# Kernel tuning notes

Hardware: AMD Instinct MI355X
Metric: run time of the kernel (lower is better)

## Reference

```python
import jax, jax.numpy as jnp
import numpy as np
from jax.ops import segment_sum

N_NODES = 50000
N_EDGES = 800000
HIDDEN = 96
N_CLASSES = 10
N_GRAPHS = 64


def gcn_conv(x, W, b, src, dst, num_nodes):
    """PyG GCNConv: symmetric-normalized aggregation with self-loops.
    out = D^{-1/2} (A + I) D^{-1/2} (x W) + b, with D the degree of A + I.
    Self-loop contribution handled analytically instead of appending edges.
    """
    ones = jnp.ones((src.shape[0],), dtype=x.dtype)
    deg = segment_sum(ones, dst, num_segments=num_nodes) + 1.0  # +1 for self-loop
    dinv = jax.lax.rsqrt(deg)
    h = x @ W  # [N, H] small GEMM
    norm = dinv[src] * dinv[dst]  # [E]
    msg = h[src] * norm[:, None]  # [E, H] dominant gather
    out = segment_sum(msg, dst, num_segments=num_nodes)  # scatter-add
    out = out + h * (dinv * dinv)[:, None]  # self-loop term
    return out + b


def setup_inputs() -> dict:
    key = jax.random.key(0)
    ks = jax.random.split(key, 12)
    x = jax.random.normal(ks[0], (N_NODES, HIDDEN), dtype=jnp.float32)
    edge_index = jax.random.randint(ks[1], (2, N_EDGES), 0, N_NODES, dtype=jnp.int64)
    batch = jnp.sort(jax.random.randint(ks[2], (N_NODES,), 0, N_GRAPHS, dtype=jnp.int64))
    s = 1.0 / np.sqrt(HIDDEN)
    W0 = jax.random.normal(ks[3], (HIDDEN, HIDDEN), dtype=jnp.float32) * s
    b0 = jnp.zeros((HIDDEN,), dtype=jnp.float32)
    W1 = jax.random.normal(ks[4], (HIDDEN, HIDDEN), dtype=jnp.float32) * s
    b1 = jnp.zeros((HIDDEN,), dtype=jnp.float32)
    W2 = jax.random.normal(ks[5], (HIDDEN, HIDDEN), dtype=jnp.float32) * s
    b2 = jnp.zeros((HIDDEN,), dtype=jnp.float32)
    W_lin = jax.random.normal(ks[6], (HIDDEN, N_CLASSES), dtype=jnp.float32) * s
    b_lin = jnp.zeros((N_CLASSES,), dtype=jnp.float32)
    return {"x": x, "edge_index": edge_index, "batch": batch,
            "W0": W0, "b0": b0, "W1": W1, "b1": b1, "W2": W2, "b2": b2,
            "W_lin": W_lin, "b_lin": b_lin}


def reference(x, edge_index, batch, W0, b0, W1, b1, W2, b2, W_lin, b_lin):
    src, dst = edge_index[0], edge_index[1]
    n = x.shape[0]
    h = jax.nn.relu(gcn_conv(x, W0, b0, src, dst, n))
    h = jax.nn.relu(gcn_conv(h, W1, b1, src, dst, n))
    h = gcn_conv(h, W2, b2, src, dst, n)  # last layer: no activation
    # global_mean_pool over batch index
    sums = segment_sum(h, batch, num_segments=N_GRAPHS)  # [G, H]
    cnts = segment_sum(jnp.ones((n,), dtype=h.dtype), batch, num_segments=N_GRAPHS)
    pooled = sums / jnp.maximum(cnts, 1.0)[:, None]
    # dropout is identity in eval mode
    return pooled @ W_lin + b_lin  # [G, num_classes]
```

## Files before the change

### kernel.cpp

```cpp
#include <hip/hip_runtime.h>
#include <hip/hip_bf16.h>

#define HID 96
#define NGRAPHS 64
#define SENT 0xC3C3u
#define NROWS 50116

typedef __attribute__((ext_vector_type(8))) short short8;
typedef __attribute__((ext_vector_type(4))) float floatx4;
typedef __attribute__((ext_vector_type(8))) unsigned short ushort8v;

__device__ __forceinline__ float bf16_to_f32(unsigned short u) {
    unsigned int v = ((unsigned int)u) << 16;
    return __builtin_bit_cast(float, v);
}
__device__ __forceinline__ unsigned short f32_to_bf16(float f) {
    unsigned int u = __builtin_bit_cast(unsigned int, f);
    u += 0x7fff + ((u >> 16) & 1);
    return (unsigned short)(u >> 16);
}

__device__ __forceinline__ void gather_batch(const unsigned short* __restrict__ h,
                                             const unsigned short* __restrict__ csr,
                                             int i, int fi, float& a0, float& a1) {
    ushort8v iv = *(const ushort8v*)(csr + i);
    ushort2 v0 = *(const ushort2*)(h + (size_t)iv[0] * HID + fi);
    ushort2 v1 = *(const ushort2*)(h + (size_t)iv[1] * HID + fi);
    ushort2 v2 = *(const ushort2*)(h + (size_t)iv[2] * HID + fi);
    ushort2 v3 = *(const ushort2*)(h + (size_t)iv[3] * HID + fi);
    ushort2 v4 = *(const ushort2*)(h + (size_t)iv[4] * HID + fi);
    ushort2 v5 = *(const ushort2*)(h + (size_t)iv[5] * HID + fi);
    ushort2 v6 = *(const ushort2*)(h + (size_t)iv[6] * HID + fi);
    ushort2 v7 = *(const ushort2*)(h + (size_t)iv[7] * HID + fi);
    a0 += bf16_to_f32(v0.x) + bf16_to_f32(v1.x) + bf16_to_f32(v2.x) +
          bf16_to_f32(v3.x) + bf16_to_f32(v4.x) + bf16_to_f32(v5.x) +
          bf16_to_f32(v6.x) + bf16_to_f32(v7.x);
    a1 += bf16_to_f32(v0.y) + bf16_to_f32(v1.y) + bf16_to_f32(v2.y) +
          bf16_to_f32(v3.y) + bf16_to_f32(v4.y) + bf16_to_f32(v5.y) +
          bf16_to_f32(v6.y) + bf16_to_f32(v7.y);
}

__device__ __forceinline__ void gather2(const unsigned short* __restrict__ h,
                                        const unsigned short* __restrict__ csr,
                                        int i0, int e0, int i1, int e1, int fi,
                                        float& a00, float& a01, float& a10,
                                        float& a11) {
    while (i0 < e0 && i1 < e1) {
        ushort8v ca = *(const ushort8v*)(csr + i0);
        ushort8v cb = *(const ushort8v*)(csr + i1);
        i0 += 8;
        i1 += 8;
        ushort2 u0 = *(const ushort2*)(h + (size_t)ca[0] * HID + fi);
        ushort2 u1 = *(const ushort2*)(h + (size_t)ca[1] * HID + fi);
        ushort2 u2 = *(const ushort2*)(h + (size_t)ca[2] * HID + fi);
        ushort2 u3 = *(const ushort2*)(h + (size_t)ca[3] * HID + fi);
        ushort2 u4 = *(const ushort2*)(h + (size_t)ca[4] * HID + fi);
        ushort2 u5 = *(const ushort2*)(h + (size_t)ca[5] * HID + fi);
        ushort2 u6 = *(const ushort2*)(h + (size_t)ca[6] * HID + fi);
        ushort2 u7 = *(const ushort2*)(h + (size_t)ca[7] * HID + fi);
        ushort2 w0 = *(const ushort2*)(h + (size_t)cb[0] * HID + fi);
        ushort2 w1 = *(const ushort2*)(h + (size_t)cb[1] * HID + fi);
        ushort2 w2 = *(const ushort2*)(h + (size_t)cb[2] * HID + fi);
        ushort2 w3 = *(const ushort2*)(h + (size_t)cb[3] * HID + fi);
        ushort2 w4 = *(const ushort2*)(h + (size_t)cb[4] * HID + fi);
        ushort2 w5 = *(const ushort2*)(h + (size_t)cb[5] * HID + fi);
        ushort2 w6 = *(const ushort2*)(h + (size_t)cb[6] * HID + fi);
        ushort2 w7 = *(const ushort2*)(h + (size_t)cb[7] * HID + fi);
        a00 += bf16_to_f32(u0.x) + bf16_to_f32(u1.x) + bf16_to_f32(u2.x) +
               bf16_to_f32(u3.x) + bf16_to_f32(u4.x) + bf16_to_f32(u5.x) +
               bf16_to_f32(u6.x) + bf16_to_f32(u7.x);
        a01 += bf16_to_f32(u0.y) + bf16_to_f32(u1.y) + bf16_to_f32(u2.y) +
               bf16_to_f32(u3.y) + bf16_to_f32(u4.y) + bf16_to_f32(u5.y) +
               bf16_to_f32(u6.y) + bf16_to_f32(u7.y);
        a10 += bf16_to_f32(w0.x) + bf16_to_f32(w1.x) + bf16_to_f32(w2.x) +
               bf16_to_f32(w3.x) + bf16_to_f32(w4.x) + bf16_to_f32(w5.x) +
               bf16_to_f32(w6.x) + bf16_to_f32(w7.x);
        a11 += bf16_to_f32(w0.y) + bf16_to_f32(w1.y) + bf16_to_f32(w2.y) +
               bf16_to_f32(w3.y) + bf16_to_f32(w4.y) + bf16_to_f32(w5.y) +
               bf16_to_f32(w6.y) + bf16_to_f32(w7.y);
    }
    for (; i0 < e0; i0 += 8) gather_batch(h, csr, i0, fi, a00, a01);
    for (; i1 < e1; i1 += 8) gather_batch(h, csr, i1, fi, a10, a11);
}

__global__ __launch_bounds__(256) void init_kernel(
    int* __restrict__ deg, float* __restrict__ psum,
    unsigned short* __restrict__ bufA, unsigned short* __restrict__ bufB, int N) {
    int i = blockIdx.x * 256 + threadIdx.x;
    if (i < N) deg[i] = 0;
    if (i < NGRAPHS * HID + NGRAPHS) psum[i] = 0.0f;
    if (i < HID) {
        bufA[(size_t)SENT * HID + i] = 0;
        bufB[(size_t)SENT * HID + i] = 0;
    }
}

__global__ void deg_kernel(const int* __restrict__ dst, int* __restrict__ deg,
                           int n_edges) {
    int t = blockIdx.x * blockDim.x + threadIdx.x;
    int e0 = t * 4;
    if (e0 + 4 <= n_edges) {
        int4 d4 = *(const int4*)(dst + e0);
        atomicAdd(&deg[d4.x], 1);
        atomicAdd(&deg[d4.y], 1);
        atomicAdd(&deg[d4.z], 1);
        atomicAdd(&deg[d4.w], 1);
    } else {
        for (int e = e0; e < n_edges; e++) atomicAdd(&deg[dst[e]], 1);
    }
}

__global__ __launch_bounds__(256) void scan_phaseA(const int* __restrict__ deg,
                                                   float* __restrict__ dinv,
                                                   int* __restrict__ blocksum,
                                                   int N) {
    int i = blockIdx.x * 256 + threadIdx.x;
    int d = (i < N) ? deg[i] : 0;
    if (i < N) dinv[i] = rsqrtf((float)d + 1.0f);
    int v = (d + 7) & ~7;
#pragma unroll
    for (int off = 32; off > 0; off >>= 1) v += __shfl_down(v, off, 64);
    __shared__ int s[4];
    if ((threadIdx.x & 63) == 0) s[threadIdx.x >> 6] = v;
    __syncthreads();
    if (threadIdx.x == 0) blocksum[blockIdx.x] = s[0] + s[1] + s[2] + s[3];
}

__global__ __launch_bounds__(256) void scan_phaseC(const int* __restrict__ deg,
                                                   const int* __restrict__ blocksum,
                                                   int* __restrict__ rowptr,
                                                   int* __restrict__ cursor,
                                                   int N, int NB) {
    int t = threadIdx.x;
    int mine = (t < NB && t < blockIdx.x) ? blocksum[t] : 0;
#pragma unroll
    for (int off = 32; off > 0; off >>= 1) mine += __shfl_down(mine, off, 64);
    __shared__ int ps[4];
    if ((t & 63) == 0) ps[t >> 6] = mine;
    __syncthreads();
    int pref = ps[0] + ps[1] + ps[2] + ps[3];

    __shared__ int s[256];
    int i = blockIdx.x * 256 + t;
    int own = (i < N) ? (deg[i] + 7) & ~7 : 0;
    s[t] = own;
    __syncthreads();
#pragma unroll
    for (int off = 1; off < 256; off <<= 1) {
        int v = (t >= off) ? s[t - off] : 0;
        __syncthreads();
        s[t] += v;
        __syncthreads();
    }
    if (i < N) {
        int r = pref + s[t] - own;
        rowptr[i] = r;
        cursor[i] = r;
        if (i == N - 1) rowptr[N] = r + own;
    }
}

__global__ void csr_fill(const int* __restrict__ src, const int* __restrict__ dst,
                         int* __restrict__ cursor,
                         unsigned short* __restrict__ csr_src, int n_edges) {
    int t = blockIdx.x * blockDim.x + threadIdx.x;
    int e0 = t * 8;
    if (e0 + 8 <= n_edges) {
        int4 da = *(const int4*)(dst + e0);
        int4 db = *(const int4*)(dst + e0 + 4);
        int4 sa = *(const int4*)(src + e0);
        int4 sb = *(const int4*)(src + e0 + 4);
        int p0 = atomicAdd(&cursor[da.x], 1);
        int p1 = atomicAdd(&cursor[da.y], 1);
        int p2 = atomicAdd(&cursor[da.z], 1);
        int p3 = atomicAdd(&cursor[da.w], 1);
        int p4 = atomicAdd(&cursor[db.x], 1);
        int p5 = atomicAdd(&cursor[db.y], 1);
        int p6 = atomicAdd(&cursor[db.z], 1);
        int p7 = atomicAdd(&cursor[db.w], 1);
        csr_src[p0] = (unsigned short)sa.x;
        csr_src[p1] = (unsigned short)sa.y;
        csr_src[p2] = (unsigned short)sa.z;
        csr_src[p3] = (unsigned short)sa.w;
        csr_src[p4] = (unsigned short)sb.x;
        csr_src[p5] = (unsigned short)sb.y;
        csr_src[p6] = (unsigned short)sb.z;
        csr_src[p7] = (unsigned short)sb.w;
    } else {
        for (int e = e0; e < n_edges; e++) {
            int p = atomicAdd(&cursor[dst[e]], 1);
            csr_src[p] = (unsigned short)src[e];
        }
    }
}

__global__ void swizzle_W(const float* __restrict__ W0, const float* __restrict__ W1,
                          const float* __restrict__ W2, unsigned short* __restrict__ Wz) {
    const float* W = (blockIdx.x == 0) ? W0 : (blockIdx.x == 1) ? W1 : W2;
    unsigned short* dst = Wz + blockIdx.x * HID * HID;
    for (int e = threadIdx.x; e < HID * HID; e += blockDim.x) {
        int k = e / HID, n = e % HID;
        int nt = n >> 4, kki = k >> 5, quad = (k >> 3) & 3, j = k & 7;
        int lane = (n & 15) | (quad << 4);
        dst[(((nt * 3 + kki) * 64 + lane) << 3) | j] = f32_to_bf16(W[e]);
    }
}

__global__ __launch_bounds__(256) void gemm0_f32(
    const float* __restrict__ X, const unsigned short* __restrict__ Wz,
    const float* __restrict__ dinv, unsigned short* __restrict__ Out, int Mtiles) {
    int wv = threadIdx.x >> 6;
    int lane = threadIdx.x & 63;
    int quad = lane >> 4;
    int mrow = lane & 15;
    int tt = blockIdx.x * 2 + (wv >> 1);
    int half = wv & 1;
    if (tt >= Mtiles) return;

    short8 bfrag[9];
    const short8* Wz8 = (const short8*)Wz;
#pragma unroll
    for (int f = 0; f < 9; f++) bfrag[f] = Wz8[(half * 9 + f) * 64 + lane];

    int m0 = tt * 16;
    const float* arow = X + (size_t)(m0 + mrow) * HID + quad * 8;
    short8 a[3];
#pragma unroll
    for (int kb = 0; kb < 3; kb++) {
        float4 u = *(const float4*)(arow + kb * 32);
        float4 v = *(const float4*)(arow + kb * 32 + 4);
        short8 t;
        t[0] = (short)f32_to_bf16(u.x); t[1] = (short)f32_to_bf16(u.y);
        t[2] = (short)f32_to_bf16(u.z); t[3] = (short)f32_to_bf16(u.w);
        t[4] = (short)f32_to_bf16(v.x); t[5] = (short)f32_to_bf16(v.y);
        t[6] = (short)f32_to_bf16(v.z); t[7] = (short)f32_to_bf16(v.w);
        a[kb] = t;
    }
    float dscale[4];
#pragma unroll
    for (int r = 0; r < 4; r++) dscale[r] = dinv[m0 + quad * 4 + r];
    unsigned short* orow = Out + (size_t)m0 * HID;
#pragma unroll
    for (int ntl = 0; ntl < 3; ntl++) {
        int nt = half * 3 + ntl;
        floatx4 c = {0.0f, 0.0f, 0.0f, 0.0f};
        c = __builtin_amdgcn_mfma_f32_16x16x32_bf16(a[0], bfrag[ntl * 3 + 0], c, 0, 0, 0);
        c = __builtin_amdgcn_mfma_f32_16x16x32_bf16(a[1], bfrag[ntl * 3 + 1], c, 0, 0, 0);
        c = __builtin_amdgcn_mfma_f32_16x16x32_bf16(a[2], bfrag[ntl * 3 + 2], c, 0, 0, 0);
#pragma unroll
        for (int r = 0; r < 4; r++)
            orow[(size_t)(quad * 4 + r) * HID + nt * 16 + mrow] =
                f32_to_bf16(c[r] * dscale[r]);
    }
}

__global__ __launch_bounds__(256) void fused_gather_gemm(
    const unsigned short* __restrict__ h, const int* __restrict__ rowptr,
    const unsigned short* __restrict__ csr, const float* __restrict__ dinv,
    const float* __restrict__ bias, const unsigned short* __restrict__ Wz,
    unsigned short* __restrict__ Out, int Mtiles) {
    __shared__ unsigned short tile[2][16][104];
    int wv = threadIdx.x >> 6;
    int lane = threadIdx.x & 63;
    int quad = lane >> 4;
    int mrow = lane & 15;
    int tsel = wv >> 1;
    int half = wv & 1;
    int tt = blockIdx.x * 2 + tsel;
    bool active = tt < Mtiles;
    int fi = (lane < 48) ? lane * 2 : 94;

    if (active) {
        float b0 = bias[fi], b1 = bias[fi + 1];
        int n0 = tt * 16;
        for (int jj = 0; jj < 8; jj += 2) {
            int j0 = half * 8 + jj;
            int na = n0 + j0;
            int nb = na + 1;
            int ia = rowptr[na];
            int ea = rowptr[na + 1];
            int ib = ea;
            int eb = rowptr[nb + 1];
            float da = dinv[na], db = dinv[nb];
            ushort2 ha = *(const ushort2*)(h + (size_t)na * HID + fi);
            ushort2 hb = *(const ushort2*)(h + (size_t)nb * HID + fi);
            float a00 = bf16_to_f32(ha.x), a01 = bf16_to_f32(ha.y);
            float a10 = bf16_to_f32(hb.x), a11 = bf16_to_f32(hb.y);
            gather2(h, csr, ia, ea, ib, eb, fi, a00, a01, a10, a11);
            a00 = fmaxf(a00 * da + b0, 0.0f);
            a01 = fmaxf(a01 * da + b1, 0.0f);
            a10 = fmaxf(a10 * db + b0, 0.0f);
            a11 = fmaxf(a11 * db + b1, 0.0f);
            if (lane < 48) {
                tile[tsel][j0][fi] = f32_to_bf16(a00);
                tile[tsel][j0][fi + 1] = f32_to_bf16(a01);
                tile[tsel][j0 + 1][fi] = f32_to_bf16(a10);
                tile[tsel][j0 + 1][fi + 1] = f32_to_bf16(a11);
            }
        }
    }
    __syncthreads();
    if (!active) return;

    short8 bfrag[9];
    const short8* Wz8 = (const short8*)Wz;
#pragma unroll
    for (int f = 0; f < 9; f++) bfrag[f] = Wz8[(half * 9 + f) * 64 + lane];

    const unsigned short* tp = &tile[tsel][0][0];
    short8 a[3];
#pragma unroll
    for (int kb = 0; kb < 3; kb++)
        a[kb] = *(const short8*)(tp + mrow * 104 + quad * 8 + kb * 32);
    int n0 = tt * 16;
    float dscale[4];
#pragma unroll
    for (int r = 0; r < 4; r++) dscale[r] = dinv[n0 + quad * 4 + r];
    unsigned short* orow = Out + (size_t)n0 * HID;
#pragma unroll
    for (int ntl = 0; ntl < 3; ntl++) {
        int nt = half * 3 + ntl;
        floatx4 c = {0.0f, 0.0f, 0.0f, 0.0f};
        c = __builtin_amdgcn_mfma_f32_16x16x32_bf16(a[0], bfrag[ntl * 3 + 0], c, 0, 0, 0);
        c = __builtin_amdgcn_mfma_f32_16x16x32_bf16(a[1], bfrag[ntl * 3 + 1], c, 0, 0, 0);
        c = __builtin_amdgcn_mfma_f32_16x16x32_bf16(a[2], bfrag[ntl * 3 + 2], c, 0, 0, 0);
#pragma unroll
        for (int r = 0; r < 4; r++)
            orow[(size_t)(quad * 4 + r) * HID + nt * 16 + mrow] =
                f32_to_bf16(c[r] * dscale[r]);
    }
}

__global__ __launch_bounds__(256) void gather_pool(
    const unsigned short* __restrict__ h, const int* __restrict__ rowptr,
    const unsigned short* __restrict__ csr, const float* __restrict__ dinv,
    const float* __restrict__ bias, const int* __restrict__ batch,
    float* __restrict__ psum, float* __restrict__ pcnt, int Ntiles8) {
    int wv = threadIdx.x >> 6;
    int lane = threadIdx.x & 63;
    int tt = blockIdx.x * 4 + wv;
    if (tt >= Ntiles8) return;
    int fi = (lane < 48) ? lane * 2 : 94;
    float b0 = bias[fi], b1 = bias[fi + 1];

    int n0 = tt * 8;
    int g_cur = batch[n0];
    float s0 = 0.0f, s1 = 0.0f;
    int cnt = 0;
    for (int jj = 0; jj < 8; jj += 2) {
        int na = n0 + jj;
        int nb = na + 1;
        int ia = rowptr[na];
        int ea = rowptr[na + 1];
        int ib = ea;
        int eb = rowptr[nb + 1];
        float da = dinv[na], db = dinv[nb];
        ushort2 ha = *(const ushort2*)(h + (size_t)na * HID + fi);
        ushort2 hb = *(const ushort2*)(h + (size_t)nb * HID + fi);
        float a00 = bf16_to_f32(ha.x), a01 = bf16_to_f32(ha.y);
        float a10 = bf16_to_f32(hb.x), a11 = bf16_to_f32(hb.y);
        gather2(h, csr, ia, ea, ib, eb, fi, a00, a01, a10, a11);
        a00 = a00 * da + b0;
        a01 = a01 * da + b1;
        a10 = a10 * db + b0;
        a11 = a11 * db + b1;
        int ga = batch[na];
        if (ga != g_cur) {
            if (lane < 48) {
                atomicAdd(&psum[g_cur * HID + fi], s0);
                atomicAdd(&psum[g_cur * HID + fi + 1], s1);
            }
            if (lane == 0) atomicAdd(&pcnt[g_cur], (float)cnt);
            s0 = 0.0f; s1 = 0.0f; cnt = 0;
            g_cur = ga;
        }
        s0 += a00; s1 += a01; cnt++;
        int gb = batch[nb];
        if (gb != g_cur) {
            if (lane < 48) {
                atomicAdd(&psum[g_cur * HID + fi], s0);
                atomicAdd(&psum[g_cur * HID + fi + 1], s1);
            }
            if (lane == 0) atomicAdd(&pcnt[g_cur], (float)cnt);
            s0 = 0.0f; s1 = 0.0f; cnt = 0;
            g_cur = gb;
        }
        s0 += a10; s1 += a11; cnt++;
    }
    if (lane < 48) {
        atomicAdd(&psum[g_cur * HID + fi], s0);
        atomicAdd(&psum[g_cur * HID + fi + 1], s1);
    }
    if (lane == 0) atomicAdd(&pcnt[g_cur], (float)cnt);
}

__global__ __launch_bounds__(640) void final_kernel(
    const float* __restrict__ sums, const float* __restrict__ cnts,
    const float* __restrict__ Wlin, const float* __restrict__ blin,
    float* __restrict__ out) {
    int t = threadIdx.x;
    if (t >= NGRAPHS * 10) return;
    int g = t / 10;
    int c = t % 10;
    float denom = fmaxf(cnts[g], 1.0f);
    float acc = blin[c];
#pragma unroll
    for (int f = 0; f < HID; f++)
        acc += (sums[g * HID + f] / denom) * Wlin[f * 10 + c];
    out[t] = acc;
}

extern "C" void kernel_launch(void* const* d_in, const int* in_sizes, int n_in,
                              void* d_out, int out_size, void* d_ws,
                              size_t ws_size, hipStream_t stream) {
    const float* x = (const float*)d_in[0];
    const int* edge = (const int*)d_in[1];
    const int* batch = (const int*)d_in[2];
    const float* W[3] = {(const float*)d_in[3], (const float*)d_in[5],
                         (const float*)d_in[7]};
    const float* B[3] = {(const float*)d_in[4], (const float*)d_in[6],
                         (const float*)d_in[8]};
    const float* Wlin = (const float*)d_in[9];
    const float* blin = (const float*)d_in[10];
    float* out = (float*)d_out;

    int N = in_sizes[0] / HID;
    int E = in_sizes[1] / 2;
    const int* src = edge;
    const int* dst = edge + E;
    int NB = (N + 255) / 256;

    char* ws = (char*)d_ws;
    size_t off = 0;
    auto alloc = [&](size_t bytes) {
        void* p = ws + off;
        off += (bytes + 255) & ~(size_t)255;
        return p;
    };
    int* deg = (int*)alloc((size_t)N * 4);
    float* dinv = (float*)alloc((size_t)N * 4);
    int* rowptr = (int*)alloc(((size_t)N + 1) * 4);
    int* cursor = (int*)alloc((size_t)N * 4);
    int* blocksum = (int*)alloc((size_t)NB * 4);
    size_t csr_cap = (size_t)E + 8 * (size_t)N;
    unsigned short* csr_src = (unsigned short*)alloc(csr_cap * 2 + 64);
    unsigned short* Wz = (unsigned short*)alloc(3 * HID * HID * 2);
    unsigned short* bufA = (unsigned short*)alloc((size_t)NROWS * HID * 2);
    unsigned short* bufB = (unsigned short*)alloc((size_t)NROWS * HID * 2);
    float* psum = (float*)alloc((NGRAPHS * HID + NGRAPHS) * 4);
    float* pcnt = psum + NGRAPHS * HID;

    hipMemsetAsync(csr_src, 0xC3, csr_cap * 2, stream);
    init_kernel<<<NB, 256, 0, stream>>>(deg, psum, bufA, bufB, N);
    deg_kernel<<<(E / 4 + 255) / 256, 256, 0, stream>>>(dst, deg, E);
    scan_phaseA<<<NB, 256, 0, stream>>>(deg, dinv, blocksum, N);
    scan_phaseC<<<NB, 256, 0, stream>>>(deg, blocksum, rowptr, cursor, N, NB);
    csr_fill<<<(E / 8 + 255) / 256, 256, 0, stream>>>(src, dst, cursor, csr_src, E);
    swizzle_W<<<3, 256, 0, stream>>>(W[0], W[1], W[2], Wz);

    int Mtiles = (N + 15) / 16;
    int grid2 = (Mtiles + 1) / 2;
    int Ntiles8 = (N + 7) / 8;
    int gridp = (Ntiles8 + 3) / 4;

    gemm0_f32<<<grid2, 256, 0, stream>>>(x, Wz, dinv, bufA, Mtiles);
    fused_gather_gemm<<<grid2, 256, 0, stream>>>(
        bufA, rowptr, csr_src, dinv, B[0], Wz + 1 * HID * HID, bufB, Mtiles);
    fused_gather_gemm<<<grid2, 256, 0, stream>>>(
        bufB, rowptr, csr_src, dinv, B[1], Wz + 2 * HID * HID, bufA, Mtiles);
    gather_pool<<<gridp, 256, 0, stream>>>(bufA, rowptr, csr_src, dinv, B[2],
                                           batch, psum, pcnt, Ntiles8);
    final_kernel<<<1, 640, 0, stream>>>(psum, pcnt, Wlin, blin, out);
}
```

Baseline: 307.8 us.

## Slice feature buffers into 12-column panels and split gather from GEMM

Stores the bf16 node features as 8 column slices of 12 features each (slice-major), so each gather block works on one slice of about 1.2 MB that can stay cache-resident during the random neighbour gather. The fused gather+GEMM and gather+pool kernels become separate gather_sliced, gemm_sliced and pool_sliced kernels. The aim is a better cache hit rate for the irregular row accesses. In exchange there are more launches, the CSR indices are read 8 times, and intermediate activations make an extra round trip through memory.

```diff
diff --git a/kernel.cpp b/kernel.cpp
--- a/kernel.cpp
+++ b/kernel.cpp
@@ -5,6 +5,7 @@
 #define NGRAPHS 64
 #define SENT 0xC3C3u
 #define NROWS 50116
+#define NPB 84
 
 typedef __attribute__((ext_vector_type(8))) short short8;
 typedef __attribute__((ext_vector_type(4))) float floatx4;
@@ -18,69 +19,6 @@
     unsigned int u = __builtin_bit_cast(unsigned int, f);
     u += 0x7fff + ((u >> 16) & 1);
     return (unsigned short)(u >> 16);
-}
-
-__device__ __forceinline__ void gather_batch(const unsigned short* __restrict__ h,
-                                             const unsigned short* __restrict__ csr,
-                                             int i, int fi, float& a0, float& a1) {
-    ushort8v iv = *(const ushort8v*)(csr + i);
-    ushort2 v0 = *(const ushort2*)(h + (size_t)iv[0] * HID + fi);
-    ushort2 v1 = *(const ushort2*)(h + (size_t)iv[1] * HID + fi);
-    ushort2 v2 = *(const ushort2*)(h + (size_t)iv[2] * HID + fi);
-    ushort2 v3 = *(const ushort2*)(h + (size_t)iv[3] * HID + fi);
-    ushort2 v4 = *(const ushort2*)(h + (size_t)iv[4] * HID + fi);
-    ushort2 v5 = *(const ushort2*)(h + (size_t)iv[5] * HID + fi);
-    ushort2 v6 = *(const ushort2*)(h + (size_t)iv[6] * HID + fi);
-    ushort2 v7 = *(const ushort2*)(h + (size_t)iv[7] * HID + fi);
-    a0 += bf16_to_f32(v0.x) + bf16_to_f32(v1.x) + bf16_to_f32(v2.x) +
-          bf16_to_f32(v3.x) + bf16_to_f32(v4.x) + bf16_to_f32(v5.x) +
-          bf16_to_f32(v6.x) + bf16_to_f32(v7.x);
-    a1 += bf16_to_f32(v0.y) + bf16_to_f32(v1.y) + bf16_to_f32(v2.y) +
-          bf16_to_f32(v3.y) + bf16_to_f32(v4.y) + bf16_to_f32(v5.y) +
-          bf16_to_f32(v6.y) + bf16_to_f32(v7.y);
-}
-
-__device__ __forceinline__ void gather2(const unsigned short* __restrict__ h,
-                                        const unsigned short* __restrict__ csr,
-                                        int i0, int e0, int i1, int e1, int fi,
-                                        float& a00, float& a01, float& a10,
-                                        float& a11) {
-    while (i0 < e0 && i1 < e1) {
-        ushort8v ca = *(const ushort8v*)(csr + i0);
-        ushort8v cb = *(const ushort8v*)(csr + i1);
-        i0 += 8;
-        i1 += 8;
-        ushort2 u0 = *(const ushort2*)(h + (size_t)ca[0] * HID + fi);
-        ushort2 u1 = *(const ushort2*)(h + (size_t)ca[1] * HID + fi);
-        ushort2 u2 = *(const ushort2*)(h + (size_t)ca[2] * HID + fi);
-        ushort2 u3 = *(const ushort2*)(h + (size_t)ca[3] * HID + fi);
-        ushort2 u4 = *(const ushort2*)(h + (size_t)ca[4] * HID + fi);
-        ushort2 u5 = *(const ushort2*)(h + (size_t)ca[5] * HID + fi);
-        ushort2 u6 = *(const ushort2*)(h + (size_t)ca[6] * HID + fi);
-        ushort2 u7 = *(const ushort2*)(h + (size_t)ca[7] * HID + fi);
-        ushort2 w0 = *(const ushort2*)(h + (size_t)cb[0] * HID + fi);
-        ushort2 w1 = *(const ushort2*)(h + (size_t)cb[1] * HID + fi);
-        ushort2 w2 = *(const ushort2*)(h + (size_t)cb[2] * HID + fi);
-        ushort2 w3 = *(const ushort2*)(h + (size_t)cb[3] * HID + fi);
-        ushort2 w4 = *(const ushort2*)(h + (size_t)cb[4] * HID + fi);
-        ushort2 w5 = *(const ushort2*)(h + (size_t)cb[5] * HID + fi);
-        ushort2 w6 = *(const ushort2*)(h + (size_t)cb[6] * HID + fi);
-        ushort2 w7 = *(const ushort2*)(h + (size_t)cb[7] * HID + fi);
-        a00 += bf16_to_f32(u0.x) + bf16_to_f32(u1.x) + bf16_to_f32(u2.x) +
-               bf16_to_f32(u3.x) + bf16_to_f32(u4.x) + bf16_to_f32(u5.x) +
-               bf16_to_f32(u6.x) + bf16_to_f32(u7.x);
-        a01 += bf16_to_f32(u0.y) + bf16_to_f32(u1.y) + bf16_to_f32(u2.y) +
-               bf16_to_f32(u3.y) + bf16_to_f32(u4.y) + bf16_to_f32(u5.y) +
-               bf16_to_f32(u6.y) + bf16_to_f32(u7.y);
-        a10 += bf16_to_f32(w0.x) + bf16_to_f32(w1.x) + bf16_to_f32(w2.x) +
-               bf16_to_f32(w3.x) + bf16_to_f32(w4.x) + bf16_to_f32(w5.x) +
-               bf16_to_f32(w6.x) + bf16_to_f32(w7.x);
-        a11 += bf16_to_f32(w0.y) + bf16_to_f32(w1.y) + bf16_to_f32(w2.y) +
-               bf16_to_f32(w3.y) + bf16_to_f32(w4.y) + bf16_to_f32(w5.y) +
-               bf16_to_f32(w6.y) + bf16_to_f32(w7.y);
-    }
-    for (; i0 < e0; i0 += 8) gather_batch(h, csr, i0, fi, a00, a01);
-    for (; i1 < e1; i1 += 8) gather_batch(h, csr, i1, fi, a10, a11);
 }
 
 __global__ __launch_bounds__(256) void init_kernel(
@@ -90,8 +28,9 @@
     if (i < N) deg[i] = 0;
     if (i < NGRAPHS * HID + NGRAPHS) psum[i] = 0.0f;
     if (i < HID) {
-        bufA[(size_t)SENT * HID + i] = 0;
-        bufB[(size_t)SENT * HID + i] = 0;
+        size_t off = ((size_t)(i / 12) * NROWS + SENT) * 12 + (i % 12);
+        bufA[off] = 0;
+        bufB[off] = 0;
     }
 }
 
@@ -239,7 +178,6 @@
     float dscale[4];
 #pragma unroll
     for (int r = 0; r < 4; r++) dscale[r] = dinv[m0 + quad * 4 + r];
-    unsigned short* orow = Out + (size_t)m0 * HID;
 #pragma unroll
     for (int ntl = 0; ntl < 3; ntl++) {
         int nt = half * 3 + ntl;
@@ -247,76 +185,47 @@
         c = __builtin_amdgcn_mfma_f32_16x16x32_bf16(a[0], bfrag[ntl * 3 + 0], c, 0, 0, 0);
         c = __builtin_amdgcn_mfma_f32_16x16x32_bf16(a[1], bfrag[ntl * 3 + 1], c, 0, 0, 0);
         c = __builtin_amdgcn_mfma_f32_16x16x32_bf16(a[2], bfrag[ntl * 3 + 2], c, 0, 0, 0);
+        int f = nt * 16 + mrow;
+        unsigned short* ocol = Out + (size_t)(f / 12) * NROWS * 12 + (f % 12);
 #pragma unroll
         for (int r = 0; r < 4; r++)
-            orow[(size_t)(quad * 4 + r) * HID + nt * 16 + mrow] =
-                f32_to_bf16(c[r] * dscale[r]);
-    }
-}
-
-__global__ __launch_bounds__(256) void fused_gather_gemm(
-    const unsigned short* __restrict__ h, const int* __restrict__ rowptr,
-    const unsigned short* __restrict__ csr, const float* __restrict__ dinv,
-    const float* __restrict__ bias, const unsigned short* __restrict__ Wz,
-    unsigned short* __restrict__ Out, int Mtiles) {
-    __shared__ unsigned short tile[2][16][104];
+            ocol[(size_t)(m0 + quad * 4 + r) * 12] = f32_to_bf16(c[r] * dscale[r]);
+    }
+}
+
+__global__ __launch_bounds__(256) void gemm_sliced(
+    const unsigned short* __restrict__ A, const unsigned short* __restrict__ Wz,
+    const float* __restrict__ dinv, unsigned short* __restrict__ Out, int Mtiles) {
     int wv = threadIdx.x >> 6;
     int lane = threadIdx.x & 63;
     int quad = lane >> 4;
     int mrow = lane & 15;
-    int tsel = wv >> 1;
+    int tt = blockIdx.x * 2 + (wv >> 1);
     int half = wv & 1;
-    int tt = blockIdx.x * 2 + tsel;
-    bool active = tt < Mtiles;
-    int fi = (lane < 48) ? lane * 2 : 94;
-
-    if (active) {
-        float b0 = bias[fi], b1 = bias[fi + 1];
-        int n0 = tt * 16;
-        for (int jj = 0; jj < 8; jj += 2) {
-            int j0 = half * 8 + jj;
-            int na = n0 + j0;
-            int nb = na + 1;
-            int ia = rowptr[na];
-            int ea = rowptr[na + 1];
-            int ib = ea;
-            int eb = rowptr[nb + 1];
-            float da = dinv[na], db = dinv[nb];
-            ushort2 ha = *(const ushort2*)(h + (size_t)na * HID + fi);
-            ushort2 hb = *(const ushort2*)(h + (size_t)nb * HID + fi);
-            float a00 = bf16_to_f32(ha.x), a01 = bf16_to_f32(ha.y);
-            float a10 = bf16_to_f32(hb.x), a11 = bf16_to_f32(hb.y);
-            gather2(h, csr, ia, ea, ib, eb, fi, a00, a01, a10, a11);
-            a00 = fmaxf(a00 * da + b0, 0.0f);
-            a01 = fmaxf(a01 * da + b1, 0.0f);
-            a10 = fmaxf(a10 * db + b0, 0.0f);
-            a11 = fmaxf(a11 * db + b1, 0.0f);
-            if (lane < 48) {
-                tile[tsel][j0][fi] = f32_to_bf16(a00);
-                tile[tsel][j0][fi + 1] = f32_to_bf16(a01);
-                tile[tsel][j0 + 1][fi] = f32_to_bf16(a10);
-                tile[tsel][j0 + 1][fi + 1] = f32_to_bf16(a11);
-            }
-        }
-    }
-    __syncthreads();
-    if (!active) return;
+    if (tt >= Mtiles) return;
 
     short8 bfrag[9];
     const short8* Wz8 = (const short8*)Wz;
 #pragma unroll
     for (int f = 0; f < 9; f++) bfrag[f] = Wz8[(half * 9 + f) * 64 + lane];
 
-    const unsigned short* tp = &tile[tsel][0][0];
+    int m0 = tt * 16;
+    int m = m0 + mrow;
     short8 a[3];
 #pragma unroll
-    for (int kb = 0; kb < 3; kb++)
-        a[kb] = *(const short8*)(tp + mrow * 104 + quad * 8 + kb * 32);
-    int n0 = tt * 16;
+    for (int kb = 0; kb < 3; kb++) {
+        int c = quad * 8 + kb * 32;
+        int c4 = c + 4;
+        ushort4 lo = *(const ushort4*)(A + ((size_t)(c / 12) * NROWS + m) * 12 + (c % 12));
+        ushort4 hi = *(const ushort4*)(A + ((size_t)(c4 / 12) * NROWS + m) * 12 + (c4 % 12));
+        short8 t;
+        t[0] = (short)lo.x; t[1] = (short)lo.y; t[2] = (short)lo.z; t[3] = (short)lo.w;
+        t[4] = (short)hi.x; t[5] = (short)hi.y; t[6] = (short)hi.z; t[7] = (short)hi.w;
+        a[kb] = t;
+    }
     float dscale[4];
 #pragma unroll
-    for (int r = 0; r < 4; r++) dscale[r] = dinv[n0 + quad * 4 + r];
-    unsigned short* orow = Out + (size_t)n0 * HID;
+    for (int r = 0; r < 4; r++) dscale[r] = dinv[m0 + quad * 4 + r];
 #pragma unroll
     for (int ntl = 0; ntl < 3; ntl++) {
         int nt = half * 3 + ntl;
@@ -324,74 +233,116 @@
         c = __builtin_amdgcn_mfma_f32_16x16x32_bf16(a[0], bfrag[ntl * 3 + 0], c, 0, 0, 0);
         c = __builtin_amdgcn_mfma_f32_16x16x32_bf16(a[1], bfrag[ntl * 3 + 1], c, 0, 0, 0);
         c = __builtin_amdgcn_mfma_f32_16x16x32_bf16(a[2], bfrag[ntl * 3 + 2], c, 0, 0, 0);
+        int f = nt * 16 + mrow;
+        unsigned short* ocol = Out + (size_t)(f / 12) * NROWS * 12 + (f % 12);
 #pragma unroll
         for (int r = 0; r < 4; r++)
-            orow[(size_t)(quad * 4 + r) * HID + nt * 16 + mrow] =
-                f32_to_bf16(c[r] * dscale[r]);
-    }
-}
-
-__global__ __launch_bounds__(256) void gather_pool(
+            ocol[(size_t)(m0 + quad * 4 + r) * 12] = f32_to_bf16(c[r] * dscale[r]);
+    }
+}
+
+__global__ __launch_bounds__(256) void gather_sliced(
     const unsigned short* __restrict__ h, const int* __restrict__ rowptr,
     const unsigned short* __restrict__ csr, const float* __restrict__ dinv,
-    const float* __restrict__ bias, const int* __restrict__ batch,
-    float* __restrict__ psum, float* __restrict__ pcnt, int Ntiles8) {
+    const float* __restrict__ bias, unsigned short* __restrict__ outa,
+    int N, int do_relu) {
+    int s = blockIdx.x & 7;
+    int tile = blockIdx.x >> 3;
     int wv = threadIdx.x >> 6;
     int lane = threadIdx.x & 63;
-    int tt = blockIdx.x * 4 + wv;
-    if (tt >= Ntiles8) return;
-    int fi = (lane < 48) ? lane * 2 : 94;
-    float b0 = bias[fi], b1 = bias[fi + 1];
-
-    int n0 = tt * 8;
-    int g_cur = batch[n0];
-    float s0 = 0.0f, s1 = 0.0f;
-    int cnt = 0;
-    for (int jj = 0; jj < 8; jj += 2) {
-        int na = n0 + jj;
-        int nb = na + 1;
-        int ia = rowptr[na];
-        int ea = rowptr[na + 1];
-        int ib = ea;
-        int eb = rowptr[nb + 1];
-        float da = dinv[na], db = dinv[nb];
-        ushort2 ha = *(const ushort2*)(h + (size_t)na * HID + fi);
-        ushort2 hb = *(const ushort2*)(h + (size_t)nb * HID + fi);
-        float a00 = bf16_to_f32(ha.x), a01 = bf16_to_f32(ha.y);
-        float a10 = bf16_to_f32(hb.x), a11 = bf16_to_f32(hb.y);
-        gather2(h, csr, ia, ea, ib, eb, fi, a00, a01, a10, a11);
-        a00 = a00 * da + b0;
-        a01 = a01 * da + b1;
-        a10 = a10 * db + b0;
-        a11 = a11 * db + b1;
-        int ga = batch[na];
-        if (ga != g_cur) {
-            if (lane < 48) {
-                atomicAdd(&psum[g_cur * HID + fi], s0);
-                atomicAdd(&psum[g_cur * HID + fi + 1], s1);
-            }
-            if (lane == 0) atomicAdd(&pcnt[g_cur], (float)cnt);
-            s0 = 0.0f; s1 = 0.0f; cnt = 0;
-            g_cur = ga;
+    int sub = lane / 3;
+    int r = lane - sub * 3;
+    if (sub >= 21) return;
+    int n = tile * NPB + wv * 21 + sub;
+    if (n >= N) return;
+
+    const unsigned short* hs = h + (size_t)s * NROWS * 12;
+    int fo = r * 4;
+    int start = rowptr[n];
+    int end = rowptr[n + 1];
+    float di = dinv[n];
+
+    ushort4 hv = *(const ushort4*)(hs + (size_t)n * 12 + fo);
+    float a0 = bf16_to_f32(hv.x), a1 = bf16_to_f32(hv.y);
+    float a2 = bf16_to_f32(hv.z), a3 = bf16_to_f32(hv.w);
+
+    for (int i = start; i < end; i += 8) {
+        ushort8v iv = *(const ushort8v*)(csr + i);
+        ushort4 v0 = *(const ushort4*)(hs + (size_t)iv[0] * 12 + fo);
+        ushort4 v1 = *(const ushort4*)(hs + (size_t)iv[1] * 12 + fo);
+        ushort4 v2 = *(const ushort4*)(hs + (size_t)iv[2] * 12 + fo);
+        ushort4 v3 = *(const ushort4*)(hs + (size_t)iv[3] * 12 + fo);
+        ushort4 v4 = *(const ushort4*)(hs + (size_t)iv[4] * 12 + fo);
+        ushort4 v5 = *(const ushort4*)(hs + (size_t)iv[5] * 12 + fo);
+        ushort4 v6 = *(const ushort4*)(hs + (size_t)iv[6] * 12 + fo);
+        ushort4 v7 = *(const ushort4*)(hs + (size_t)iv[7] * 12 + fo);
+        a0 += bf16_to_f32(v0.x) + bf16_to_f32(v1.x) + bf16_to_f32(v2.x) +
+              bf16_to_f32(v3.x) + bf16_to_f32(v4.x) + bf16_to_f32(v5.x) +
+              bf16_to_f32(v6.x) + bf16_to_f32(v7.x);
+        a1 += bf16_to_f32(v0.y) + bf16_to_f32(v1.y) + bf16_to_f32(v2.y) +
+              bf16_to_f32(v3.y) + bf16_to_f32(v4.y) + bf16_to_f32(v5.y) +
+              bf16_to_f32(v6.y) + bf16_to_f32(v7.y);
+        a2 += bf16_to_f32(v0.z) + bf16_to_f32(v1.z) + bf16_to_f32(v2.z) +
+              bf16_to_f32(v3.z) + bf16_to_f32(v4.z) + bf16_to_f32(v5.z) +
+              bf16_to_f32(v6.z) + bf16_to_f32(v7.z);
+        a3 += bf16_to_f32(v0.w) + bf16_to_f32(v1.w) + bf16_to_f32(v2.w) +
+              bf16_to_f32(v3.w) + bf16_to_f32(v4.w) + bf16_to_f32(v5.w) +
+              bf16_to_f32(v6.w) + bf16_to_f32(v7.w);
+    }
+    float4 bb = *(const float4*)(bias + s * 12 + fo);
+    a0 = a0 * di + bb.x;
+    a1 = a1 * di + bb.y;
+    a2 = a2 * di + bb.z;
+    a3 = a3 * di + bb.w;
+    if (do_relu) {
+        a0 = fmaxf(a0, 0.0f);
+        a1 = fmaxf(a1, 0.0f);
+        a2 = fmaxf(a2, 0.0f);
+        a3 = fmaxf(a3, 0.0f);
+    }
+    ushort4 o;
+    o.x = f32_to_bf16(a0);
+    o.y = f32_to_bf16(a1);
+    o.z = f32_to_bf16(a2);
+    o.w = f32_to_bf16(a3);
+    *(ushort4*)(outa + (size_t)s * NROWS * 12 + (size_t)n * 12 + fo) = o;
+}
+
+#define PCH 32
+__global__ __launch_bounds__(96) void pool_sliced(
+    const unsigned short* __restrict__ a3, const int* __restrict__ batch,
+    float* __restrict__ sums, float* __restrict__ cnts, int N) {
+    int n0 = blockIdx.x * PCH;
+    if (n0 >= N) return;
+    int f = threadIdx.x;
+    const unsigned short* col = a3 + (size_t)(f / 12) * NROWS * 12 + (f % 12);
+    int nend = min(n0 + PCH, N);
+    int gfirst = batch[n0];
+    int glast = batch[nend - 1];
+    if (gfirst == glast) {
+        float acc = 0.0f;
+#pragma unroll 8
+        for (int n = n0; n < nend; n++) acc += bf16_to_f32(col[(size_t)n * 12]);
+        atomicAdd(&sums[gfirst * HID + f], acc);
+        if (f == 0) atomicAdd(&cnts[gfirst], (float)(nend - n0));
+        return;
+    }
+    int g_cur = gfirst;
+    float acc = 0.0f, cacc = 0.0f;
+    for (int n = n0; n < nend; n++) {
+        int g = batch[n];
+        if (g != g_cur) {
+            atomicAdd(&sums[g_cur * HID + f], acc);
+            if (f == 0) atomicAdd(&cnts[g_cur], cacc);
+            acc = 0.0f;
+            cacc = 0.0f;
+            g_cur = g;
         }
-        s0 += a00; s1 += a01; cnt++;
-        int gb = batch[nb];
-        if (gb != g_cur) {
-            if (lane < 48) {
-                atomicAdd(&psum[g_cur * HID + fi], s0);
-                atomicAdd(&psum[g_cur * HID + fi + 1], s1);
-            }
-            if (lane == 0) atomicAdd(&pcnt[g_cur], (float)cnt);
-            s0 = 0.0f; s1 = 0.0f; cnt = 0;
-            g_cur = gb;
-        }
-        s0 += a10; s1 += a11; cnt++;
-    }
-    if (lane < 48) {
-        atomicAdd(&psum[g_cur * HID + fi], s0);
-        atomicAdd(&psum[g_cur * HID + fi + 1], s1);
-    }
-    if (lane == 0) atomicAdd(&pcnt[g_cur], (float)cnt);
+        acc += bf16_to_f32(col[(size_t)n * 12]);
+        cacc += 1.0f;
+    }
+    atomicAdd(&sums[g_cur * HID + f], acc);
+    if (f == 0) atomicAdd(&cnts[g_cur], cacc);
 }
 
 __global__ __launch_bounds__(640) void final_kernel(
@@ -460,15 +411,21 @@
 
     int Mtiles = (N + 15) / 16;
     int grid2 = (Mtiles + 1) / 2;
-    int Ntiles8 = (N + 7) / 8;
-    int gridp = (Ntiles8 + 3) / 4;
+    int gtiles = (N + NPB - 1) / NPB;
+    int ggrid = 8 * gtiles;
+    int pgrid = (N + PCH - 1) / PCH;
 
     gemm0_f32<<<grid2, 256, 0, stream>>>(x, Wz, dinv, bufA, Mtiles);
-    fused_gather_gemm<<<grid2, 256, 0, stream>>>(
-        bufA, rowptr, csr_src, dinv, B[0], Wz + 1 * HID * HID, bufB, Mtiles);
-    fused_gather_gemm<<<grid2, 256, 0, stream>>>(
-        bufB, rowptr, csr_src, dinv, B[1], Wz + 2 * HID * HID, bufA, Mtiles);
-    gather_pool<<<gridp, 256, 0, stream>>>(bufA, rowptr, csr_src, dinv, B[2],
-                                           batch, psum, pcnt, Ntiles8);
+    gather_sliced<<<ggrid, 256, 0, stream>>>(bufA, rowptr, csr_src, dinv, B[0],
+                                             bufB, N, 1);
+    gemm_sliced<<<grid2, 256, 0, stream>>>(bufB, Wz + 1 * HID * HID, dinv, bufA,
+                                           Mtiles);
+    gather_sliced<<<ggrid, 256, 0, stream>>>(bufA, rowptr, csr_src, dinv, B[1],
+                                             bufB, N, 1);
+    gemm_sliced<<<grid2, 256, 0, stream>>>(bufB, Wz + 2 * HID * HID, dinv, bufA,
+                                           Mtiles);
+    gather_sliced<<<ggrid, 256, 0, stream>>>(bufA, rowptr, csr_src, dinv, B[2],
+                                             bufB, N, 0);
+    pool_sliced<<<pgrid, 96, 0, stream>>>(bufB, batch, psum, pcnt, N);
     final_kernel<<<1, 640, 0, stream>>>(psum, pcnt, Wlin, blin, out);
 }
```

New measurement: 344.2 us. +11.8%, slower.

## Feature-slice last-layer features per XCC for cache-local gather-pool

Applied to the files above, without the earlier changes.

The second fused layer now writes its output in a sliced layout: eight column slices of 12 features, each stored contiguously over all rows. The final gather+pool kernel becomes a persistent kernel with per-slice atomic work queues. Each block starts on the slice matching its XCC ID so that slice's working set (about 1.2 MB) stays in that XCC's L2, and gathers 8-byte feature chunks per neighbor. This targets the random-gather L2 miss traffic, at the cost of eight passes over the CSR and rowptr, more atomics into psum, and strided scattered writes in the layer-2 epilogue.

```diff
diff --git a/kernel.cpp b/kernel.cpp
--- a/kernel.cpp
+++ b/kernel.cpp
@@ -5,6 +5,7 @@
 #define NGRAPHS 64
 #define SENT 0xC3C3u
 #define NROWS 50116
+#define NPT 1344
 
 typedef __attribute__((ext_vector_type(8))) short short8;
 typedef __attribute__((ext_vector_type(4))) float floatx4;
@@ -84,14 +85,17 @@
 }
 
 __global__ __launch_bounds__(256) void init_kernel(
-    int* __restrict__ deg, float* __restrict__ psum,
-    unsigned short* __restrict__ bufA, unsigned short* __restrict__ bufB, int N) {
+    int* __restrict__ deg, float* __restrict__ psum, int* __restrict__ queues,
+    unsigned short* __restrict__ bufA, unsigned short* __restrict__ bufB,
+    unsigned short* __restrict__ bufC, int N) {
     int i = blockIdx.x * 256 + threadIdx.x;
     if (i < N) deg[i] = 0;
     if (i < NGRAPHS * HID + NGRAPHS) psum[i] = 0.0f;
+    if (i < 8) queues[i] = 0;
     if (i < HID) {
         bufA[(size_t)SENT * HID + i] = 0;
         bufB[(size_t)SENT * HID + i] = 0;
+        bufC[((size_t)(i / 12) * NROWS + SENT) * 12 + (i % 12)] = 0;
     }
 }
 
@@ -258,7 +262,7 @@
     const unsigned short* __restrict__ h, const int* __restrict__ rowptr,
     const unsigned short* __restrict__ csr, const float* __restrict__ dinv,
     const float* __restrict__ bias, const unsigned short* __restrict__ Wz,
-    unsigned short* __restrict__ Out, int Mtiles) {
+    unsigned short* __restrict__ Out, int Mtiles, int sliced_out) {
     __shared__ unsigned short tile[2][16][104];
     int wv = threadIdx.x >> 6;
     int lane = threadIdx.x & 63;
@@ -316,7 +320,6 @@
     float dscale[4];
 #pragma unroll
     for (int r = 0; r < 4; r++) dscale[r] = dinv[n0 + quad * 4 + r];
-    unsigned short* orow = Out + (size_t)n0 * HID;
 #pragma unroll
     for (int ntl = 0; ntl < 3; ntl++) {
         int nt = half * 3 + ntl;
@@ -324,74 +327,116 @@
         c = __builtin_amdgcn_mfma_f32_16x16x32_bf16(a[0], bfrag[ntl * 3 + 0], c, 0, 0, 0);
         c = __builtin_amdgcn_mfma_f32_16x16x32_bf16(a[1], bfrag[ntl * 3 + 1], c, 0, 0, 0);
         c = __builtin_amdgcn_mfma_f32_16x16x32_bf16(a[2], bfrag[ntl * 3 + 2], c, 0, 0, 0);
-#pragma unroll
-        for (int r = 0; r < 4; r++)
-            orow[(size_t)(quad * 4 + r) * HID + nt * 16 + mrow] =
-                f32_to_bf16(c[r] * dscale[r]);
-    }
-}
-
-__global__ __launch_bounds__(256) void gather_pool(
+        int f = nt * 16 + mrow;
+        if (sliced_out) {
+            unsigned short* ocol = Out + ((size_t)(f / 12) * NROWS) * 12 + (f % 12);
+#pragma unroll
+            for (int r = 0; r < 4; r++)
+                ocol[(size_t)(n0 + quad * 4 + r) * 12] = f32_to_bf16(c[r] * dscale[r]);
+        } else {
+            unsigned short* orow = Out + (size_t)n0 * HID;
+#pragma unroll
+            for (int r = 0; r < 4; r++)
+                orow[(size_t)(quad * 4 + r) * HID + f] = f32_to_bf16(c[r] * dscale[r]);
+        }
+    }
+}
+
+__global__ __launch_bounds__(256) void gather_pool_sliced(
     const unsigned short* __restrict__ h, const int* __restrict__ rowptr,
     const unsigned short* __restrict__ csr, const float* __restrict__ dinv,
     const float* __restrict__ bias, const int* __restrict__ batch,
-    float* __restrict__ psum, float* __restrict__ pcnt, int Ntiles8) {
+    float* __restrict__ psum, float* __restrict__ pcnt,
+    int* __restrict__ queues, int N, int Ntiles) {
+    int xcc;
+    asm volatile("s_getreg_b32 %0, hwreg(HW_REG_XCC_ID)" : "=s"(xcc));
+    xcc &= 7;
+    __shared__ int tile_s;
     int wv = threadIdx.x >> 6;
     int lane = threadIdx.x & 63;
-    int tt = blockIdx.x * 4 + wv;
-    if (tt >= Ntiles8) return;
-    int fi = (lane < 48) ? lane * 2 : 94;
-    float b0 = bias[fi], b1 = bias[fi + 1];
-
-    int n0 = tt * 8;
-    int g_cur = batch[n0];
-    float s0 = 0.0f, s1 = 0.0f;
-    int cnt = 0;
-    for (int jj = 0; jj < 8; jj += 2) {
-        int na = n0 + jj;
-        int nb = na + 1;
-        int ia = rowptr[na];
-        int ea = rowptr[na + 1];
-        int ib = ea;
-        int eb = rowptr[nb + 1];
-        float da = dinv[na], db = dinv[nb];
-        ushort2 ha = *(const ushort2*)(h + (size_t)na * HID + fi);
-        ushort2 hb = *(const ushort2*)(h + (size_t)nb * HID + fi);
-        float a00 = bf16_to_f32(ha.x), a01 = bf16_to_f32(ha.y);
-        float a10 = bf16_to_f32(hb.x), a11 = bf16_to_f32(hb.y);
-        gather2(h, csr, ia, ea, ib, eb, fi, a00, a01, a10, a11);
-        a00 = a00 * da + b0;
-        a01 = a01 * da + b1;
-        a10 = a10 * db + b0;
-        a11 = a11 * db + b1;
-        int ga = batch[na];
-        if (ga != g_cur) {
-            if (lane < 48) {
-                atomicAdd(&psum[g_cur * HID + fi], s0);
-                atomicAdd(&psum[g_cur * HID + fi + 1], s1);
+    int sub = lane / 3;
+    int r = lane - sub * 3;
+    bool alive = (sub < 21);
+    int fo = r * 4;
+
+    for (int pass = 0; pass < 8; pass++) {
+        int q = (xcc + pass) & 7;
+        const unsigned short* hs = h + (size_t)q * NROWS * 12;
+        float4 bb4 = *(const float4*)(bias + q * 12 + fo);
+        while (true) {
+            if (threadIdx.x == 0) tile_s = atomicAdd(&queues[q], 1);
+            __syncthreads();
+            int tile = tile_s;
+            __syncthreads();
+            if (tile >= Ntiles) break;
+            if (alive) {
+                int base = tile * NPT + wv * 336 + sub * 16;
+                float r0 = 0, r1 = 0, r2 = 0, r3 = 0;
+                int g_cur = -1, cnt = 0;
+                for (int k = 0; k < 16; k++) {
+                    int n = base + k;
+                    if (n >= N) break;
+                    int start = rowptr[n];
+                    int end = rowptr[n + 1];
+                    float di = dinv[n];
+                    ushort4 hv = *(const ushort4*)(hs + (size_t)n * 12 + fo);
+                    float a0 = bf16_to_f32(hv.x), a1 = bf16_to_f32(hv.y);
+                    float a2 = bf16_to_f32(hv.z), a3 = bf16_to_f32(hv.w);
+                    for (int i = start; i < end; i += 8) {
+                        ushort8v iv = *(const ushort8v*)(csr + i);
+                        ushort4 v0 = *(const ushort4*)(hs + (size_t)iv[0] * 12 + fo);
+                        ushort4 v1 = *(const ushort4*)(hs + (size_t)iv[1] * 12 + fo);
+                        ushort4 v2 = *(const ushort4*)(hs + (size_t)iv[2] * 12 + fo);
+                        ushort4 v3 = *(const ushort4*)(hs + (size_t)iv[3] * 12 + fo);
+                        ushort4 v4 = *(const ushort4*)(hs + (size_t)iv[4] * 12 + fo);
+                        ushort4 v5 = *(const ushort4*)(hs + (size_t)iv[5] * 12 + fo);
+                        ushort4 v6 = *(const ushort4*)(hs + (size_t)iv[6] * 12 + fo);
+                        ushort4 v7 = *(const ushort4*)(hs + (size_t)iv[7] * 12 + fo);
+                        a0 += bf16_to_f32(v0.x) + bf16_to_f32(v1.x) + bf16_to_f32(v2.x) +
+                              bf16_to_f32(v3.x) + bf16_to_f32(v4.x) + bf16_to_f32(v5.x) +
+                              bf16_to_f32(v6.x) + bf16_to_f32(v7.x);
+                        a1 += bf16_to_f32(v0.y) + bf16_to_f32(v1.y) + bf16_to_f32(v2.y) +
+                              bf16_to_f32(v3.y) + bf16_to_f32(v4.y) + bf16_to_f32(v5.y) +
+                              bf16_to_f32(v6.y) + bf16_to_f32(v7.y);
+                        a2 += bf16_to_f32(v0.z) + bf16_to_f32(v1.z) + bf16_to_f32(v2.z) +
+                              bf16_to_f32(v3.z) + bf16_to_f32(v4.z) + bf16_to_f32(v5.z) +
+                              bf16_to_f32(v6.z) + bf16_to_f32(v7.z);
+                        a3 += bf16_to_f32(v0.w) + bf16_to_f32(v1.w) + bf16_to_f32(v2.w) +
+                              bf16_to_f32(v3.w) + bf16_to_f32(v4.w) + bf16_to_f32(v5.w) +
+                              bf16_to_f32(v6.w) + bf16_to_f32(v7.w);
+                    }
+                    a0 = a0 * di + bb4.x;
+                    a1 = a1 * di + bb4.y;
+                    a2 = a2 * di + bb4.z;
+                    a3 = a3 * di + bb4.w;
+                    int g = batch[n];
+                    if (g != g_cur) {
+                        if (cnt > 0) {
+                            float* p = &psum[g_cur * HID + q * 12 + fo];
+                            atomicAdd(p + 0, r0);
+                            atomicAdd(p + 1, r1);
+                            atomicAdd(p + 2, r2);
+                            atomicAdd(p + 3, r3);
+                            if (q == 0 && r == 0) atomicAdd(&pcnt[g_cur], (float)cnt);
+                        }
+                        r0 = r1 = r2 = r3 = 0.0f;
+                        cnt = 0;
+                        g_cur = g;
+                    }
+                    r0 += a0; r1 += a1; r2 += a2; r3 += a3;
+                    cnt++;
+                }
+                if (cnt > 0) {
+                    float* p = &psum[g_cur * HID + q * 12 + fo];
+                    atomicAdd(p + 0, r0);
+                    atomicAdd(p + 1, r1);
+                    atomicAdd(p + 2, r2);
+                    atomicAdd(p + 3, r3);
+                    if (q == 0 && r == 0) atomicAdd(&pcnt[g_cur], (float)cnt);
+                }
             }
-            if (lane == 0) atomicAdd(&pcnt[g_cur], (float)cnt);
-            s0 = 0.0f; s1 = 0.0f; cnt = 0;
-            g_cur = ga;
         }
-        s0 += a00; s1 += a01; cnt++;
-        int gb = batch[nb];
-        if (gb != g_cur) {
-            if (lane < 48) {
-                atomicAdd(&psum[g_cur * HID + fi], s0);
-                atomicAdd(&psum[g_cur * HID + fi + 1], s1);
-            }
-            if (lane == 0) atomicAdd(&pcnt[g_cur], (float)cnt);
-            s0 = 0.0f; s1 = 0.0f; cnt = 0;
-            g_cur = gb;
-        }
-        s0 += a10; s1 += a11; cnt++;
-    }
-    if (lane < 48) {
-        atomicAdd(&psum[g_cur * HID + fi], s0);
-        atomicAdd(&psum[g_cur * HID + fi + 1], s1);
-    }
-    if (lane == 0) atomicAdd(&pcnt[g_cur], (float)cnt);
+    }
 }
 
 __global__ __launch_bounds__(640) void final_kernel(
@@ -442,16 +487,18 @@
     int* rowptr = (int*)alloc(((size_t)N + 1) * 4);
     int* cursor = (int*)alloc((size_t)N * 4);
     int* blocksum = (int*)alloc((size_t)NB * 4);
+    int* queues = (int*)alloc(8 * 4);
     size_t csr_cap = (size_t)E + 8 * (size_t)N;
     unsigned short* csr_src = (unsigned short*)alloc(csr_cap * 2 + 64);
     unsigned short* Wz = (unsigned short*)alloc(3 * HID * HID * 2);
     unsigned short* bufA = (unsigned short*)alloc((size_t)NROWS * HID * 2);
     unsigned short* bufB = (unsigned short*)alloc((size_t)NROWS * HID * 2);
+    unsigned short* bufC = (unsigned short*)alloc((size_t)NROWS * HID * 2);
     float* psum = (float*)alloc((NGRAPHS * HID + NGRAPHS) * 4);
     float* pcnt = psum + NGRAPHS * HID;
 
     hipMemsetAsync(csr_src, 0xC3, csr_cap * 2, stream);
-    init_kernel<<<NB, 256, 0, stream>>>(deg, psum, bufA, bufB, N);
+    init_kernel<<<NB, 256, 0, stream>>>(deg, psum, queues, bufA, bufB, bufC, N);
     deg_kernel<<<(E / 4 + 255) / 256, 256, 0, stream>>>(dst, deg, E);
     scan_phaseA<<<NB, 256, 0, stream>>>(deg, dinv, blocksum, N);
     scan_phaseC<<<NB, 256, 0, stream>>>(deg, blocksum, rowptr, cursor, N, NB);
@@ -460,15 +507,15 @@
 
     int Mtiles = (N + 15) / 16;
     int grid2 = (Mtiles + 1) / 2;
-    int Ntiles8 = (N + 7) / 8;
-    int gridp = (Ntiles8 + 3) / 4;
+    int Ntiles = (N + NPT - 1) / NPT;
 
     gemm0_f32<<<grid2, 256, 0, stream>>>(x, Wz, dinv, bufA, Mtiles);
     fused_gather_gemm<<<grid2, 256, 0, stream>>>(
-        bufA, rowptr, csr_src, dinv, B[0], Wz + 1 * HID * HID, bufB, Mtiles);
+        bufA, rowptr, csr_src, dinv, B[0], Wz + 1 * HID * HID, bufB, Mtiles, 0);
     fused_gather_gemm<<<grid2, 256, 0, stream>>>(
-        bufB, rowptr, csr_src, dinv, B[1], Wz + 2 * HID * HID, bufA, Mtiles);
-    gather_pool<<<gridp, 256, 0, stream>>>(bufA, rowptr, csr_src, dinv, B[2],
-                                           batch, psum, pcnt, Ntiles8);
+        bufB, rowptr, csr_src, dinv, B[1], Wz + 2 * HID * HID, bufC, Mtiles, 1);
+    gather_pool_sliced<<<512, 256, 0, stream>>>(bufC, rowptr, csr_src, dinv,
+                                                B[2], batch, psum, pcnt,
+                                                queues, N, Ntiles);
     final_kernel<<<1, 640, 0, stream>>>(psum, pcnt, Wlin, blin, out);
 }
```

Result: slower. 356.2 us (+15.7%).
